# Performance work log

Measured on AMD Instinct MI355X. Metric: run time of the kernel, lower is better.

## Reference

```python
import jax, jax.numpy as jnp
import numpy as np

MSG_DIM = 100
REG_WEIGHT = 1.0
N_NODES = 100000
N_EDGES = 1000000
D_FEAT = 6
HIDDEN = 300
OUT_DIM = 2


def setup_inputs() -> dict:
    key = jax.random.key(0)
    ks = jax.random.split(key, 10)
    def glorot(k, shape):
        fan_in = shape[0]
        return jax.random.normal(k, shape, dtype=jnp.float32) / jnp.sqrt(jnp.float32(fan_in))
    return {
        "x": jax.random.normal(ks[0], (N_NODES, D_FEAT), dtype=jnp.float32),
        "edge_index": jax.random.randint(ks[1], (2, N_EDGES), 0, N_NODES, dtype=jnp.int64)
            if jax.config.jax_enable_x64 else jax.random.randint(ks[1], (2, N_EDGES), 0, N_NODES, dtype=jnp.int32),
        "y": jax.random.normal(ks[2], (N_NODES, OUT_DIM), dtype=jnp.float32),
        "target": jax.random.normal(ks[3], (N_NODES, OUT_DIM), dtype=jnp.float32),
        "W1": glorot(ks[4], (2 * D_FEAT, HIDDEN)),
        "b1": jnp.zeros((HIDDEN,), dtype=jnp.float32),
        "W2": glorot(ks[5], (HIDDEN, HIDDEN)),
        "b2": jnp.zeros((HIDDEN,), dtype=jnp.float32),
        "W3": glorot(ks[6], (HIDDEN, 2 * MSG_DIM)),
        "b3": jnp.zeros((2 * MSG_DIM,), dtype=jnp.float32),
    }


def reference(x, edge_index, y, target, W1, b1, W2, b2, W3, b3):
    # MAE term: sum |y - target| / n_nodes
    base_loss = jnp.sum(jnp.abs(y - target)) / y.shape[0]
    # Gather sender/receiver node features per edge and concat -> [E, 2*d_feat]
    e = jnp.concatenate([x[edge_index[0]], x[edge_index[1]]], axis=1)
    # edge_model MLP: 2*d_feat -> 300 -> 300 -> 2*msg_dim
    h = jax.nn.relu(e @ W1 + b1)
    h = jax.nn.relu(h @ W2 + b2)
    messages = h @ W3 + b3  # [E, 2*msg_dim]
    mu = messages[:, :MSG_DIM]
    logvar = messages[:, MSG_DIM:]
    kl_reg = jnp.sum(0.5 * (mu * mu + jnp.exp(logvar) - logvar - 1.0)) / messages.shape[0]
    return base_loss + REG_WEIGHT * kl_reg
```

## Files before the change

kernel.cpp:

```cpp
#include <hip/hip_runtime.h>

#define N_NODES 100000
#define N_EDGES 1000000
#define D_FEAT  6
#define HIDDEN  300
#define HID_P   320
#define MSG     100
#define OUTC    200
#define OUTC_P  208
#define MT      64
#define NT_H    (HID_P/16)
#define NT_M    13
#define KS_H    (HID_P/32)

typedef __bf16 bf16_t;
typedef __bf16 bf16x8 __attribute__((ext_vector_type(8)));
typedef __bf16 bf16x4 __attribute__((ext_vector_type(4)));
typedef __bf16 bf16x2 __attribute__((ext_vector_type(2)));
typedef float  floatx4 __attribute__((ext_vector_type(4)));

#define PREP_BLOCKS 700
#define LOSS_BLOCKS 200
__global__ void prep_kernel(const float* __restrict__ W1, const float* __restrict__ W2,
                            const float* __restrict__ W3, bf16_t* __restrict__ W1P,
                            bf16_t* __restrict__ W2P, bf16_t* __restrict__ W3P,
                            const float* __restrict__ y, const float* __restrict__ t,
                            float* __restrict__ out) {
    if (blockIdx.x >= PREP_BLOCKS) {
        float s = 0.f;
        for (int i = (blockIdx.x - PREP_BLOCKS) * blockDim.x + threadIdx.x;
             i < N_NODES * 2; i += LOSS_BLOCKS * blockDim.x)
            s += fabsf(y[i] - t[i]);
        #pragma unroll
        for (int off = 32; off; off >>= 1) s += __shfl_down(s, off);
        __shared__ float red[4];
        if ((threadIdx.x & 63) == 0) red[threadIdx.x >> 6] = s;
        __syncthreads();
        if (threadIdx.x == 0)
            atomicAdd(out, (red[0] + red[1] + red[2] + red[3]) * (1.0f / N_NODES));
        return;
    }
    const int n1 = NT_H * 512;
    const int n2 = NT_H * KS_H * 512;
    const int n3 = NT_M * KS_H * 512;
    const int total = n1 + n2 + n3;
    for (int id = blockIdx.x * blockDim.x + threadIdx.x; id < total;
         id += PREP_BLOCKS * blockDim.x) {
        if (id < n1) {
            int nt = id >> 9, rem = id & 511, lane = rem >> 3, j = rem & 7;
            int n = nt * 16 + (lane & 15), k = (lane >> 4) * 8 + j;
            float v = (n < HIDDEN && k < 2 * D_FEAT) ? W1[k * HIDDEN + n] : 0.f;
            W1P[id] = (bf16_t)v;
        } else if (id < n1 + n2) {
            int r = id - n1;
            int chunk = r >> 9, rem = r & 511, lane = rem >> 3, j = rem & 7;
            int ks = chunk % KS_H, nt = chunk / KS_H;
            int n = nt * 16 + (lane & 15), k = ks * 32 + (lane >> 4) * 8 + j;
            float v = (n < HIDDEN && k < HIDDEN) ? W2[k * HIDDEN + n] : 0.f;
            W2P[r] = (bf16_t)v;
        } else {
            int r = id - n1 - n2;
            int chunk = r >> 9, rem = r & 511, lane = rem >> 3, j = rem & 7;
            int ks = chunk % KS_H, nt = chunk / KS_H;
            int n = nt * 16 + (lane & 15), k = ks * 32 + (lane >> 4) * 8 + j;
            float v = (n < OUTC && k < HIDDEN) ? W3[k * OUTC + n] : 0.f;
            W3P[r] = (bf16_t)v;
        }
    }
}

static __device__ __forceinline__ floatx4 mfma16(bf16x8 a, bf16x8 b, floatx4 c) {
    return __builtin_amdgcn_mfma_f32_16x16x32_bf16(a, b, c, 0, 0, 0);
}

template<int KSN, int SE>
__device__ __forceinline__ void gemm5x4(
    const bf16_t* __restrict__ Wbase0,
    const bf16_t* __restrict__ Hsrc, int lane,
    const floatx4 (&binit)[5], floatx4 (&acc)[5][4]) {
    #pragma unroll
    for (int i = 0; i < 5; i++)
        #pragma unroll
        for (int e = 0; e < 4; e++) acc[i][e] = binit[i];
    const bf16_t* Wb = Wbase0 + lane * 8;
    const bf16_t* Hb = Hsrc + lane * 8;
    #pragma unroll 2
    for (int ks = 0; ks < KSN; ks++) {
        bf16x8 hb0 = *(const bf16x8*)(Hb + ks * 512);
        bf16x8 hb1 = *(const bf16x8*)(Hb + ks * 512 + SE);
        bf16x8 hb2 = *(const bf16x8*)(Hb + ks * 512 + 2 * SE);
        bf16x8 hb3 = *(const bf16x8*)(Hb + ks * 512 + 3 * SE);
        #pragma unroll
        for (int i = 0; i < 5; i++) {
            bf16x8 wf = *(const bf16x8*)(Wb + i * (KSN * 512) + ks * 512);
            acc[i][0] = mfma16(wf, hb0, acc[i][0]);
            acc[i][1] = mfma16(wf, hb1, acc[i][1]);
            acc[i][2] = mfma16(wf, hb2, acc[i][2]);
            acc[i][3] = mfma16(wf, hb3, acc[i][3]);
        }
    }
}

__device__ __forceinline__ void epi5(
    bf16_t* __restrict__ Hf, int w, int q, int l16, const floatx4 (&acc)[5][4]) {
    #pragma unroll
    for (int i = 0; i < 5; i++) {
        int n0 = (5 * w + i) * 16 + 4 * q;
        int ks = n0 >> 5, lp = l16 + 16 * ((n0 >> 3) & 3), j0 = n0 & 7;
        #pragma unroll
        for (int e = 0; e < 4; e++) {
            bf16x4 pk;
            #pragma unroll
            for (int r = 0; r < 4; r++)
                pk[r] = (bf16_t)fmaxf(acc[i][e][r], 0.f);
            *(bf16x4*)&Hf[((e * KS_H + ks) * 64 + lp) * 8 + j0] = pk;
        }
    }
}

__global__ __launch_bounds__(256, 3) void mlp_kernel(
    const float* __restrict__ x, const int* __restrict__ ei,
    const bf16_t* __restrict__ W1P, const bf16_t* __restrict__ W2P,
    const bf16_t* __restrict__ W3P,
    const float* __restrict__ b1, const float* __restrict__ b2,
    const float* __restrict__ b3, float* __restrict__ out) {
    __shared__ __align__(16) bf16_t A1f[4 * 64 * 8];
    __shared__ __align__(16) bf16_t Hf[4 * KS_H * 64 * 8];
    __shared__ float red[4];

    const int tid  = threadIdx.x;
    const int w    = tid >> 6, lane = tid & 63;
    const int q    = lane >> 4, l16 = lane & 15;
    const long e0 = (long)blockIdx.x * MT;

    bf16x8 wf1[5];
    floatx4 bv1[5], bv2[5];
    #pragma unroll
    for (int i = 0; i < 5; i++) {
        wf1[i] = *(const bf16x8*)&W1P[((5 * w + i) * 64 + lane) * 8];
        int n0 = (5 * w + i) * 16 + 4 * q;
        bv1[i] = (n0 < HIDDEN) ? *(const floatx4*)&b1[n0] : (floatx4){0.f, 0.f, 0.f, 0.f};
        bv2[i] = (n0 < HIDDEN) ? *(const floatx4*)&b2[n0] : (floatx4){0.f, 0.f, 0.f, 0.f};
    }

    if (tid < 2 * MT) {
        int m = tid >> 1, side = tid & 1;
        int node = ei[(long)side * N_EDGES + e0 + m];
        const float2* xr = (const float2*)(x + (long)node * D_FEAT);
        float2 v0 = xr[0], v1 = xr[1], v2 = xr[2];
        int et = m >> 4, ml = m & 15;
        bf16_t* Ab = &A1f[(et * 64 + ml) * 8];
        if (side == 0) {
            bf16x4 lo = {(bf16_t)v0.x, (bf16_t)v0.y, (bf16_t)v1.x, (bf16_t)v1.y};
            *(bf16x4*)&Ab[0] = lo;
            bf16x2 mid = {(bf16_t)v2.x, (bf16_t)v2.y};
            *(bf16x2*)&Ab[4] = mid;
        } else {
            bf16x2 hi2 = {(bf16_t)v0.x, (bf16_t)v0.y};
            *(bf16x2*)&Ab[6] = hi2;
            bf16x8 top = {(bf16_t)v1.x, (bf16_t)v1.y, (bf16_t)v2.x, (bf16_t)v2.y,
                          (bf16_t)0.f, (bf16_t)0.f, (bf16_t)0.f, (bf16_t)0.f};
            *(bf16x8*)&A1f[(et * 64 + ml + 16) * 8] = top;
        }
    } else {
        int idx = tid - 128;
        int et = idx >> 5, lr = 32 + (idx & 31);
        bf16x8 z = {};
        *(bf16x8*)&A1f[(et * 64 + lr) * 8] = z;
    }
    __syncthreads();

    floatx4 acc[5][4];

    {
        bf16x8 hb0 = *(const bf16x8*)&A1f[lane * 8];
        bf16x8 hb1 = *(const bf16x8*)&A1f[(64 + lane) * 8];
        bf16x8 hb2 = *(const bf16x8*)&A1f[(128 + lane) * 8];
        bf16x8 hb3 = *(const bf16x8*)&A1f[(192 + lane) * 8];
        #pragma unroll
        for (int i = 0; i < 5; i++) {
            acc[i][0] = mfma16(wf1[i], hb0, bv1[i]);
            acc[i][1] = mfma16(wf1[i], hb1, bv1[i]);
            acc[i][2] = mfma16(wf1[i], hb2, bv1[i]);
            acc[i][3] = mfma16(wf1[i], hb3, bv1[i]);
        }
    }
    epi5(Hf, w, q, l16, acc);
    __syncthreads();

    gemm5x4<KS_H, KS_H * 512>(W2P + (5 * w) * (KS_H * 512), Hf, lane, bv2, acc);
    __syncthreads();
    epi5(Hf, w, q, l16, acc);
    __syncthreads();

    floatx4 a3[3][4], aq;
    const int n0q = 192 + 4 * q;
    {
        #pragma unroll
        for (int t = 0; t < 3; t++) {
            int n0 = (3 * w + t) * 16 + 4 * q;
            floatx4 bv = *(const floatx4*)&b3[n0];
            #pragma unroll
            for (int e = 0; e < 4; e++) a3[t][e] = bv;
        }
        aq = (n0q < OUTC) ? *(const floatx4*)&b3[n0q] : (floatx4){0.f, 0.f, 0.f, 0.f};
    }
    {
        const bf16_t* W3b = W3P + (3 * w) * (KS_H * 512) + lane * 8;
        const bf16_t* Wqb = W3P + 12 * (KS_H * 512) + lane * 8;
        const bf16_t* Hb  = Hf + lane * 8;
        const bf16_t* Hq  = Hf + w * (KS_H * 512) + lane * 8;
        #pragma unroll 2
        for (int ks = 0; ks < KS_H; ks++) {
            bf16x8 hb0 = *(const bf16x8*)(Hb + ks * 512);
            bf16x8 hb1 = *(const bf16x8*)(Hb + ks * 512 + KS_H * 512);
            bf16x8 hb2 = *(const bf16x8*)(Hb + ks * 512 + 2 * KS_H * 512);
            bf16x8 hb3 = *(const bf16x8*)(Hb + ks * 512 + 3 * KS_H * 512);
            #pragma unroll
            for (int t = 0; t < 3; t++) {
                bf16x8 wf = *(const bf16x8*)(W3b + t * (KS_H * 512) + ks * 512);
                a3[t][0] = mfma16(wf, hb0, a3[t][0]);
                a3[t][1] = mfma16(wf, hb1, a3[t][1]);
                a3[t][2] = mfma16(wf, hb2, a3[t][2]);
                a3[t][3] = mfma16(wf, hb3, a3[t][3]);
            }
            bf16x8 wq = *(const bf16x8*)(Wqb + ks * 512);
            bf16x8 hq = *(const bf16x8*)(Hq + ks * 512);
            aq = mfma16(wq, hq, aq);
        }
    }
    float sm = 0.f, se = 0.f, sv = 0.f, cnt = 0.f;
    #pragma unroll
    for (int t = 0; t < 3; t++) {
        int n0 = (3 * w + t) * 16 + 4 * q;
        if (n0 < MSG) {
            #pragma unroll
            for (int e = 0; e < 4; e++)
                #pragma unroll
                for (int r = 0; r < 4; r++) {
                    float v = a3[t][e][r];
                    sm += v * v;
                }
        } else {
            #pragma unroll
            for (int e = 0; e < 4; e++)
                #pragma unroll
                for (int r = 0; r < 4; r++) {
                    float v = a3[t][e][r];
                    se += __expf(v);
                    sv += v;
                }
            cnt += 16.f;
        }
    }
    if (n0q < OUTC) {
        #pragma unroll
        for (int r = 0; r < 4; r++) {
            float v = aq[r];
            se += __expf(v);
            sv += v;
        }
        cnt += 4.f;
    }
    float s = sm + se - sv - cnt;
    #pragma unroll
    for (int off = 32; off; off >>= 1) s += __shfl_down(s, off);
    if (lane == 0) red[w] = s;
    __syncthreads();
    if (tid == 0)
        atomicAdd(out, (red[0] + red[1] + red[2] + red[3]) * (0.5f / N_EDGES));
}

extern "C" void kernel_launch(void* const* d_in, const int* in_sizes, int n_in,
                              void* d_out, int out_size, void* d_ws, size_t ws_size,
                              hipStream_t stream) {
    const float* x      = (const float*)d_in[0];
    const int*   ei     = (const int*)d_in[1];
    const float* y      = (const float*)d_in[2];
    const float* target = (const float*)d_in[3];
    const float* W1     = (const float*)d_in[4];
    const float* b1     = (const float*)d_in[5];
    const float* W2     = (const float*)d_in[6];
    const float* b2     = (const float*)d_in[7];
    const float* W3     = (const float*)d_in[8];
    const float* b3     = (const float*)d_in[9];
    float* out = (float*)d_out;

    bf16_t* W1P = (bf16_t*)d_ws;
    bf16_t* W2P = W1P + NT_H * 512;
    bf16_t* W3P = W2P + NT_H * KS_H * 512;

    hipMemsetAsync(d_out, 0, sizeof(float), stream);
    prep_kernel<<<PREP_BLOCKS + LOSS_BLOCKS, 256, 0, stream>>>(
        W1, W2, W3, W1P, W2P, W3P, y, target, out);
    mlp_kernel<<<N_EDGES / MT, 256, 0, stream>>>(x, ei, W1P, W2P, W3P, b1, b2, b3, out);
}
```

Measured before the change: 402.3 us.

## Gather edge features into registers, fold log2e into W3, raise occupancy

```diff
diff --git a/kernel.cpp b/kernel.cpp
--- a/kernel.cpp
+++ b/kernel.cpp
@@ -12,11 +12,12 @@
 #define NT_H    (HID_P/16)
 #define NT_M    13
 #define KS_H    (HID_P/32)
+#define LOG2E   1.44269504f
+#define LN2     0.69314718f
 
 typedef __bf16 bf16_t;
 typedef __bf16 bf16x8 __attribute__((ext_vector_type(8)));
 typedef __bf16 bf16x4 __attribute__((ext_vector_type(4)));
-typedef __bf16 bf16x2 __attribute__((ext_vector_type(2)));
 typedef float  floatx4 __attribute__((ext_vector_type(4)));
 
 #define PREP_BLOCKS 700
@@ -64,6 +65,7 @@
             int ks = chunk % KS_H, nt = chunk / KS_H;
             int n = nt * 16 + (lane & 15), k = ks * 32 + (lane >> 4) * 8 + j;
             float v = (n < OUTC && k < HIDDEN) ? W3[k * OUTC + n] : 0.f;
+            if (n >= MSG) v *= LOG2E;
             W3P[r] = (bf16_t)v;
         }
     }
@@ -118,15 +120,13 @@
     }
 }
 
-__global__ __launch_bounds__(256, 3) void mlp_kernel(
+__global__ __launch_bounds__(256, 4) void mlp_kernel(
     const float* __restrict__ x, const int* __restrict__ ei,
     const bf16_t* __restrict__ W1P, const bf16_t* __restrict__ W2P,
     const bf16_t* __restrict__ W3P,
     const float* __restrict__ b1, const float* __restrict__ b2,
     const float* __restrict__ b3, float* __restrict__ out) {
-    __shared__ __align__(16) bf16_t A1f[4 * 64 * 8];
     __shared__ __align__(16) bf16_t Hf[4 * KS_H * 64 * 8];
-    __shared__ float red[4];
 
     const int tid  = threadIdx.x;
     const int w    = tid >> 6, lane = tid & 63;
@@ -134,58 +134,54 @@
     const long e0 = (long)blockIdx.x * MT;
 
     bf16x8 wf1[5];
-    floatx4 bv1[5], bv2[5];
+    floatx4 bv1[5];
     #pragma unroll
     for (int i = 0; i < 5; i++) {
         wf1[i] = *(const bf16x8*)&W1P[((5 * w + i) * 64 + lane) * 8];
         int n0 = (5 * w + i) * 16 + 4 * q;
         bv1[i] = (n0 < HIDDEN) ? *(const floatx4*)&b1[n0] : (floatx4){0.f, 0.f, 0.f, 0.f};
+    }
+
+    bf16x8 hbg[4];
+    #pragma unroll
+    for (int et = 0; et < 4; et++) {
+        bf16x8 v = {};
+        long g = e0 + et * 16 + l16;
+        if (q == 0) {
+            int si = ei[g], di = ei[N_EDGES + g];
+            const float2* xs = (const float2*)(x + (long)si * D_FEAT);
+            const float2* xd = (const float2*)(x + (long)di * D_FEAT);
+            float2 a0 = xs[0], a1 = xs[1], a2 = xs[2], c0 = xd[0];
+            v[0] = (bf16_t)a0.x; v[1] = (bf16_t)a0.y;
+            v[2] = (bf16_t)a1.x; v[3] = (bf16_t)a1.y;
+            v[4] = (bf16_t)a2.x; v[5] = (bf16_t)a2.y;
+            v[6] = (bf16_t)c0.x; v[7] = (bf16_t)c0.y;
+        } else if (q == 1) {
+            int di = ei[N_EDGES + g];
+            const float2* xd = (const float2*)(x + (long)di * D_FEAT);
+            float2 c1 = xd[1], c2 = xd[2];
+            v[0] = (bf16_t)c1.x; v[1] = (bf16_t)c1.y;
+            v[2] = (bf16_t)c2.x; v[3] = (bf16_t)c2.y;
+        }
+        hbg[et] = v;
+    }
+
+    floatx4 acc[5][4];
+
+    #pragma unroll
+    for (int i = 0; i < 5; i++) {
+        acc[i][0] = mfma16(wf1[i], hbg[0], bv1[i]);
+        acc[i][1] = mfma16(wf1[i], hbg[1], bv1[i]);
+        acc[i][2] = mfma16(wf1[i], hbg[2], bv1[i]);
+        acc[i][3] = mfma16(wf1[i], hbg[3], bv1[i]);
+    }
+    epi5(Hf, w, q, l16, acc);
+    floatx4 bv2[5];
+    #pragma unroll
+    for (int i = 0; i < 5; i++) {
+        int n0 = (5 * w + i) * 16 + 4 * q;
         bv2[i] = (n0 < HIDDEN) ? *(const floatx4*)&b2[n0] : (floatx4){0.f, 0.f, 0.f, 0.f};
     }
-
-    if (tid < 2 * MT) {
-        int m = tid >> 1, side = tid & 1;
-        int node = ei[(long)side * N_EDGES + e0 + m];
-        const float2* xr = (const float2*)(x + (long)node * D_FEAT);
-        float2 v0 = xr[0], v1 = xr[1], v2 = xr[2];
-        int et = m >> 4, ml = m & 15;
-        bf16_t* Ab = &A1f[(et * 64 + ml) * 8];
-        if (side == 0) {
-            bf16x4 lo = {(bf16_t)v0.x, (bf16_t)v0.y, (bf16_t)v1.x, (bf16_t)v1.y};
-            *(bf16x4*)&Ab[0] = lo;
-            bf16x2 mid = {(bf16_t)v2.x, (bf16_t)v2.y};
-            *(bf16x2*)&Ab[4] = mid;
-        } else {
-            bf16x2 hi2 = {(bf16_t)v0.x, (bf16_t)v0.y};
-            *(bf16x2*)&Ab[6] = hi2;
-            bf16x8 top = {(bf16_t)v1.x, (bf16_t)v1.y, (bf16_t)v2.x, (bf16_t)v2.y,
-                          (bf16_t)0.f, (bf16_t)0.f, (bf16_t)0.f, (bf16_t)0.f};
-            *(bf16x8*)&A1f[(et * 64 + ml + 16) * 8] = top;
-        }
-    } else {
-        int idx = tid - 128;
-        int et = idx >> 5, lr = 32 + (idx & 31);
-        bf16x8 z = {};
-        *(bf16x8*)&A1f[(et * 64 + lr) * 8] = z;
-    }
-    __syncthreads();
-
-    floatx4 acc[5][4];
-
-    {
-        bf16x8 hb0 = *(const bf16x8*)&A1f[lane * 8];
-        bf16x8 hb1 = *(const bf16x8*)&A1f[(64 + lane) * 8];
-        bf16x8 hb2 = *(const bf16x8*)&A1f[(128 + lane) * 8];
-        bf16x8 hb3 = *(const bf16x8*)&A1f[(192 + lane) * 8];
-        #pragma unroll
-        for (int i = 0; i < 5; i++) {
-            acc[i][0] = mfma16(wf1[i], hb0, bv1[i]);
-            acc[i][1] = mfma16(wf1[i], hb1, bv1[i]);
-            acc[i][2] = mfma16(wf1[i], hb2, bv1[i]);
-            acc[i][3] = mfma16(wf1[i], hb3, bv1[i]);
-        }
-    }
-    epi5(Hf, w, q, l16, acc);
     __syncthreads();
 
     gemm5x4<KS_H, KS_H * 512>(W2P + (5 * w) * (KS_H * 512), Hf, lane, bv2, acc);
@@ -200,10 +196,12 @@
         for (int t = 0; t < 3; t++) {
             int n0 = (3 * w + t) * 16 + 4 * q;
             floatx4 bv = *(const floatx4*)&b3[n0];
+            if (n0 >= MSG) bv = bv * LOG2E;
             #pragma unroll
             for (int e = 0; e < 4; e++) a3[t][e] = bv;
         }
-        aq = (n0q < OUTC) ? *(const floatx4*)&b3[n0q] : (floatx4){0.f, 0.f, 0.f, 0.f};
+        aq = (n0q < OUTC) ? *(const floatx4*)&b3[n0q] * LOG2E
+                          : (floatx4){0.f, 0.f, 0.f, 0.f};
     }
     {
         const bf16_t* W3b = W3P + (3 * w) * (KS_H * 512) + lane * 8;
@@ -229,7 +227,7 @@
             aq = mfma16(wq, hq, aq);
         }
     }
-    float sm = 0.f, se = 0.f, sv = 0.f, cnt = 0.f;
+    float sm = 0.f, se = 0.f, svp = 0.f, cnt = 0.f;
     #pragma unroll
     for (int t = 0; t < 3; t++) {
         int n0 = (3 * w + t) * 16 + 4 * q;
@@ -247,8 +245,8 @@
                 #pragma unroll
                 for (int r = 0; r < 4; r++) {
                     float v = a3[t][e][r];
-                    se += __expf(v);
-                    sv += v;
+                    se += __builtin_exp2f(v);
+                    svp += v;
                 }
             cnt += 16.f;
         }
@@ -257,18 +255,16 @@
         #pragma unroll
         for (int r = 0; r < 4; r++) {
             float v = aq[r];
-            se += __expf(v);
-            sv += v;
+            se += __builtin_exp2f(v);
+            svp += v;
         }
         cnt += 4.f;
     }
-    float s = sm + se - sv - cnt;
+    float s = sm + se - svp * LN2 - cnt;
     #pragma unroll
     for (int off = 32; off; off >>= 1) s += __shfl_down(s, off);
-    if (lane == 0) red[w] = s;
-    __syncthreads();
-    if (tid == 0)
-        atomicAdd(out, (red[0] + red[1] + red[2] + red[3]) * (0.5f / N_EDGES));
+    if (lane == 0)
+        atomicAdd(out, s * (0.5f / N_EDGES));
 }
 
 extern "C" void kernel_launch(void* const* d_in, const int* in_sizes, int n_in,
```

Result: slower. 905.7 us (+125.2%).
